# Kernel tuning notes

Measured on AMD Instinct MI355X. Metric: run time of the kernel, lower is better.

## Reference

```python
import jax, jax.numpy as jnp
import numpy as np
import math

B, L, D, A, VD, H = 8, 2048, 1024, 1024, 1024, 1024
EPS = 1e-5

def gelu(x):
    return 0.5 * x * (1.0 + jax.lax.erf(x / math.sqrt(2.0)))

def setup_inputs() -> dict:
    key = jax.random.key(0)
    ks = jax.random.split(key, 12)
    s = 0.02
    return {
        "Q": jax.random.normal(ks[0], (B, L, D), jnp.float32),
        "K": jax.random.normal(ks[1], (B, L, D), jnp.float32),
        "V": jax.random.normal(ks[2], (B, L, D), jnp.float32),
        "attn_mask": jax.random.randint(ks[3], (B, L, L), 0, 2, jnp.int32),
        "Wq": jax.random.normal(ks[4], (D, A), jnp.float32) * s,
        "bq": jnp.zeros((A,), jnp.float32),
        "Wk": jax.random.normal(ks[5], (D, A), jnp.float32) * s,
        "bk": jnp.zeros((A,), jnp.float32),
        "Wv": jax.random.normal(ks[6], (D, VD), jnp.float32) * s,
        "bv": jnp.zeros((VD,), jnp.float32),
        "Wo": jax.random.normal(ks[7], (VD, H), jnp.float32) * s,
        "bo": jnp.zeros((H,), jnp.float32),
        "gamma": jnp.ones((H,), jnp.float32),
        "beta": jnp.zeros((H,), jnp.float32),
    }

def reference(Q, K, V, attn_mask, Wq, bq, Wk, bk, Wv, bv, Wo, bo, gamma, beta):
    q = Q @ Wq + bq                      # [B,L,A]
    k = K @ Wk + bk                      # [B,L,A]
    scores = jnp.einsum('bqa,bka->bqk', q, k) / math.sqrt(A)
    scores = scores + attn_mask.astype(jnp.float32) * (-1e9)
    scores = jnp.swapaxes(scores, -1, -2)  # [B,Lk,Lq]; softmax over QUERY axis
    attn = jax.nn.softmax(scores, axis=-1)
    wv = V @ Wv + bv                     # [B,L,VD]
    context = jnp.einsum('bkq,bqv->bkv', attn, wv)  # [B,L,VD]
    context = gelu(context @ Wo + bo)    # [B,L,H]
    mu = jnp.mean(context, axis=-1, keepdims=True)
    var = jnp.var(context, axis=-1, keepdims=True)
    context = (context - mu) / jnp.sqrt(var + EPS) * gamma + beta
    return context, attn
```

## Files before the change

kernel.cpp:

```cpp
#include <hip/hip_runtime.h>
#include <math.h>

typedef __bf16 bf16;
typedef __bf16 bf16x8 __attribute__((ext_vector_type(8)));
typedef __bf16 bf16x4 __attribute__((ext_vector_type(4)));
typedef float f32x4 __attribute__((ext_vector_type(4)));
typedef unsigned int u32x4 __attribute__((ext_vector_type(4)));

__device__ inline void gload16(const void* g, void* l) {
  typedef __attribute__((address_space(1))) const unsigned int guint;
  typedef __attribute__((address_space(3))) unsigned int luint;
  __builtin_amdgcn_global_load_lds((guint*)g, (luint*)l, 16, 0, 0);
}

template<int BIAS_MODE, bool GELU>
__global__ __launch_bounds__(512, 2)
void bgemm8_k(const bf16* __restrict__ A, const bf16* __restrict__ A2,
              const bf16* __restrict__ B,
              const float* __restrict__ bias, const float* __restrict__ bias2,
              bf16* __restrict__ Cout, int ldc, int K,
              long sAb, long sBb, long sCb, float scale,
              int nshift, int zshift, int mper)
{
  __shared__ __align__(16) char smem[131072];
  bf16* As = (bf16*)smem;
  bf16* Bs = (bf16*)(smem + 65536);

  const int t    = threadIdx.x;
  const int i    = blockIdx.x;
  const int c    = i & 7;
  const int s    = i >> 3;
  const int zb   = c >> zshift;
  const int mchunk = c & ((1 << zshift) - 1);
  const int m_tile = mchunk * mper + (s >> nshift);
  const int n_tile = s & ((1 << nshift) - 1);
  const int m0   = m_tile << 8;
  const int n0   = n_tile << 8;

  const float* bp = (BIAS_MODE && bias2 && zb) ? bias2 : bias;

  const int wave = t >> 6;
  const int lane = t & 63;
  const int wm = wave >> 2;
  const int wn = wave & 3;
  const int fr = lane & 15;
  const int fg = lane >> 4;

  const bf16* Aroot = (A2 && zb >= 4) ? A2 : A;
  const int   za    = (A2 && zb >= 4) ? zb - 4 : zb;
  const bf16* Abase = Aroot + (size_t)za * sAb + (size_t)m0 * K;
  const bf16* Bbase = B + (size_t)zb * sBb + (size_t)n0 * K;
  size_t gOff[2];
  int    ldsOff[2];
#pragma unroll
  for (int j = 0; j < 2; ++j) {
    const int L   = j * 8192 + t * 16;
    const int row = L >> 6;
    const int gp  = (L >> 4) & 3;
    const int g   = gp ^ ((row >> 1) & 3);
    gOff[j]   = (size_t)row * K + (size_t)g * 8;
    ldsOff[j] = j * 4096 + wave * 512;
  }
  const int HMAX = (K >> 5) * 2;

  auto stage = [&](int H) {
    if (H >= HMAX) return;
    const int sl   = H >> 1;
    const int slot = sl & 3;
    const size_t kof = (size_t)sl * 32;
    if ((H & 1) == 0) {
      gload16(Abase + kof + gOff[0], As + slot * 8192 + ldsOff[0]);
      gload16(Abase + kof + gOff[1], As + slot * 8192 + ldsOff[1]);
    } else {
      gload16(Bbase + kof + gOff[0], Bs + slot * 8192 + ldsOff[0]);
      gload16(Bbase + kof + gOff[1], Bs + slot * 8192 + ldsOff[1]);
    }
  };

  const int xsw  = (fg ^ ((fr >> 1) & 3)) * 8;
  const int aoff = (wm * 128 + fr) * 32 + xsw;
  const int boff = (wn * 64 + fr) * 32 + xsw;

  f32x4 acc[8][4] = {};
  const int T = K >> 6;

  stage(0); stage(1); stage(2); stage(3); stage(4);
  asm volatile("s_waitcnt vmcnt(6)" ::: "memory");
  __builtin_amdgcn_s_barrier();

  for (int tt = 0; tt < T; ++tt) {
#pragma unroll
    for (int p = 0; p < 4; ++p) {
      const int kk   = p & 1;
      const int oh   = p >> 1;
      const int slot = (2 * tt + kk) & 3;
      bf16x8 af[4], bfv[4];
#pragma unroll
      for (int i2 = 0; i2 < 4; ++i2)
        af[i2]  = *(const bf16x8*)(As + slot * 8192 + aoff + (oh * 4 + i2) * 512);
#pragma unroll
      for (int i2 = 0; i2 < 4; ++i2)
        bfv[i2] = *(const bf16x8*)(Bs + slot * 8192 + boff + i2 * 512);
      stage(4 * tt + p + 5);
      __builtin_amdgcn_s_barrier();
      __builtin_amdgcn_s_setprio(1);
#pragma unroll
      for (int mi = 0; mi < 4; ++mi)
#pragma unroll
        for (int ni = 0; ni < 4; ++ni)
          acc[oh * 4 + mi][ni] =
            __builtin_amdgcn_mfma_f32_16x16x32_bf16(af[mi], bfv[ni], acc[oh * 4 + mi][ni], 0, 0, 0);
      __builtin_amdgcn_s_setprio(0);
      if (p == 0) {
        if (tt == T - 1) asm volatile("s_waitcnt vmcnt(0)" ::: "memory");
        else             asm volatile("s_waitcnt vmcnt(4)" ::: "memory");
      }
      if (p == 3) {
        if (tt < T - 2)       asm volatile("s_waitcnt vmcnt(6)" ::: "memory");
        else if (tt == T - 2) asm volatile("s_waitcnt vmcnt(4)" ::: "memory");
      }
      __builtin_amdgcn_s_barrier();
    }
  }

  bf16* wbuf = (bf16*)(smem + wave * 16384);
#pragma unroll
  for (int mi = 0; mi < 8; ++mi) {
#pragma unroll
    for (int ni = 0; ni < 4; ++ni) {
      const int col = n0 + wn * 64 + ni * 16 + fr;
#pragma unroll
      for (int i2 = 0; i2 < 4; ++i2) {
        const int r = mi * 16 + fg * 4 + i2;
        float v = acc[mi][ni][i2] * scale;
        if constexpr (BIAS_MODE == 1) v += bp[col];
        if constexpr (BIAS_MODE == 2) v += bp[m0 + wm * 128 + r];
        if constexpr (GELU) v = 0.5f * v * (1.0f + erff(v * 0.70710678118f));
        const int cb = ni * 32 + fr * 2;
        *(bf16*)((char*)wbuf + r * 128 + (cb ^ ((r & 7) << 4))) = (bf16)v;
      }
    }
  }
  __syncthreads();
  const int rowbase = m0 + wm * 128;
  const int colbase = n0 + wn * 64;
#pragma unroll
  for (int j = 0; j < 16; ++j) {
    const int r  = j * 8 + (lane >> 3);
    const int cg = lane & 7;
    bf16x8 val = *(const bf16x8*)((char*)wbuf + r * 128 + ((cg << 4) ^ ((r & 7) << 4)));
    *(bf16x8*)(Cout + (size_t)zb * sCb + (size_t)(rowbase + r) * ldc + colbase + cg * 8) = val;
  }
}

__global__ __launch_bounds__(256)
void pre1_k(const float* __restrict__ W0, const float* __restrict__ W1,
            const float* __restrict__ W2, const float* __restrict__ W3,
            bf16* __restrict__ wts,
            const float* __restrict__ Q, const float* __restrict__ Kin,
            bf16* __restrict__ Qb, bf16* __restrict__ Kb, long n8)
{
  __shared__ __align__(16) char sb[64 * 72 * 2];
  const int t = threadIdx.x;
  if (blockIdx.z == 0) {
    const float* Ws[4] = {W0, W1, W2, W3};
    const int wsel = blockIdx.x >> 8;
    const float* W = Ws[wsel];
    bf16* o = wts + (size_t)wsel * (1024 * 1024);
    const int c0 = (blockIdx.x & 15) * 64;
    const int r0 = ((blockIdx.x >> 4) & 15) * 64;
    bf16 (*tile)[72] = (bf16(*)[72])sb;
    {
      const int rr = t >> 2;
      const int cc = (t & 3) * 16;
      const float* src = W + (size_t)(r0 + rr) * 1024 + c0 + cc;
#pragma unroll
      for (int j = 0; j < 16; j += 4) {
        f32x4 v = __builtin_nontemporal_load((const f32x4*)(src + j));
#pragma unroll
        for (int i = 0; i < 4; ++i) tile[cc + j + i][rr] = (bf16)v[i];
      }
    }
    __syncthreads();
    {
      const int nr = t >> 2;
      const int kc = (t & 3) * 16;
      bf16* dst = o + (size_t)(c0 + nr) * 1024 + r0 + kc;
      *(bf16x8*)dst       = *(const bf16x8*)&tile[nr][kc];
      *(bf16x8*)(dst + 8) = *(const bf16x8*)&tile[nr][kc + 8];
    }
  } else {
    const float* in = (blockIdx.z == 1) ? Q : Kin;
    bf16* out = (blockIdx.z == 1) ? Qb : Kb;
    for (long i = blockIdx.x * 256 + t; i < n8; i += (long)gridDim.x * 256) {
      f32x4 a = __builtin_nontemporal_load((const f32x4*)(in + i * 8));
      f32x4 b = __builtin_nontemporal_load((const f32x4*)(in + i * 8 + 4));
      bf16x8 o;
#pragma unroll
      for (int j = 0; j < 4; ++j) { o[j] = (bf16)a[j]; o[4 + j] = (bf16)b[j]; }
      *(bf16x8*)(out + i * 8) = o;
    }
  }
}

__global__ __launch_bounds__(256)
void pre2_k(const unsigned int* __restrict__ mask, unsigned char* __restrict__ mTb,
            const float* __restrict__ V, bf16* __restrict__ Vb, long n8)
{
  __shared__ __align__(16) char sb[64 * 72 * 2];
  const int t = threadIdx.x;
  if (blockIdx.z < 8) {
    const int b  = blockIdx.z;
    const int k0 = (blockIdx.x & 31) * 64;
    const int q0 = (blockIdx.x >> 5) * 64;
    signed char (*tile)[65] = (signed char(*)[65])sb;
    {
      const int iq = t >> 2;
      const int ic = (t & 3) * 16;
      const unsigned int* src = mask + ((size_t)b * 2048 + q0 + iq) * 2048 + k0 + ic;
#pragma unroll
      for (int j = 0; j < 16; j += 4) {
        u32x4 v = __builtin_nontemporal_load((const u32x4*)(src + j));
#pragma unroll
        for (int i = 0; i < 4; ++i) tile[ic + j + i][iq] = (signed char)v[i];
      }
    }
    __syncthreads();
    {
      const int ik = t >> 2;
      const int iq = (t & 3) * 16;
      unsigned int bits = 0;
#pragma unroll
      for (int j = 0; j < 16; ++j) bits |= (unsigned int)(tile[ik][iq + j] & 1) << j;
      *(unsigned short*)(mTb + ((size_t)b * 2048 + k0 + ik) * 256 + ((q0 + iq) >> 3)) =
          (unsigned short)bits;
    }
  } else {
    for (long i = blockIdx.x * 256 + t; i < n8; i += (long)gridDim.x * 256) {
      f32x4 a = __builtin_nontemporal_load((const f32x4*)(V + i * 8));
      f32x4 b = __builtin_nontemporal_load((const f32x4*)(V + i * 8 + 4));
      bf16x8 o;
#pragma unroll
      for (int j = 0; j < 4; ++j) { o[j] = (bf16)a[j]; o[4 + j] = (bf16)b[j]; }
      *(bf16x8*)(Vb + i * 8) = o;
    }
  }
}

__global__ __launch_bounds__(256)
void softmax_rows_k(float* __restrict__ P, const unsigned char* __restrict__ mTb,
                    bf16* __restrict__ Pb0, bf16* __restrict__ Pb1)
{
  const int b  = blockIdx.x & 7;
  const int rw = blockIdx.x >> 3;
  const size_t r = (size_t)b * 2048 + rw;
  char* slot = (char*)P + r * 8192;
  const bf16* pin = (const bf16*)slot;
  float* pout = (float*)slot;
  bf16* pb = (b < 4) ? (Pb0 + ((size_t)b * 2048 + rw) * 2048)
                     : (Pb1 + ((size_t)(b - 4) * 2048 + rw) * 2048);
  const int t = threadIdx.x;
  const int wave = t >> 6, lane = t & 63;
  bf16x8 raw = *(const bf16x8*)(pin + t * 8);
  const unsigned int mbyte = mTb[r * 256 + t];
  float v[8];
#pragma unroll
  for (int j = 0; j < 8; ++j)
    v[j] = (float)raw[j] + (((mbyte >> j) & 1) ? -1e9f : 0.0f);
  float m = -3e38f;
#pragma unroll
  for (int j = 0; j < 8; ++j) m = fmaxf(m, v[j]);
#pragma unroll
  for (int off = 32; off; off >>= 1) m = fmaxf(m, __shfl_xor(m, off));
  __shared__ float red[8];
  if (lane == 0) red[wave] = m;
  __syncthreads();
  m = fmaxf(fmaxf(red[0], red[1]), fmaxf(red[2], red[3]));
  float s = 0.0f;
#pragma unroll
  for (int j = 0; j < 8; ++j) { v[j] = __expf(v[j] - m); s += v[j]; }
#pragma unroll
  for (int off = 32; off; off >>= 1) s += __shfl_xor(s, off);
  if (lane == 0) red[4 + wave] = s;
  __syncthreads();
  s = red[4] + red[5] + red[6] + red[7];
  const float inv = 1.0f / s;
  f32x4 o0, o1;
  bf16x8 ob;
#pragma unroll
  for (int j = 0; j < 4; ++j) {
    o0[j] = v[j] * inv; o1[j] = v[4 + j] * inv;
    ob[j] = (bf16)o0[j]; ob[4 + j] = (bf16)o1[j];
  }
  __builtin_nontemporal_store(o0, (f32x4*)(pout + t * 8));
  __builtin_nontemporal_store(o1, (f32x4*)(pout + t * 8 + 4));
  *(bf16x8*)(pb + t * 8) = ob;
}

__global__ __launch_bounds__(256)
void ln_k(const bf16* __restrict__ g, const float* __restrict__ gamma,
          const float* __restrict__ beta, float* __restrict__ out)
{
  const size_t r = (size_t)(blockIdx.x & 7) * 2048 + (blockIdx.x >> 3);
  const bf16* p = g + r * 1024;
  const int t = threadIdx.x;
  const int wave = t >> 6, lane = t & 63;
  bf16x4 raw = *(const bf16x4*)(p + t * 4);
  f32x4 v;
#pragma unroll
  for (int j = 0; j < 4; ++j) v[j] = (float)raw[j];
  float s = v[0] + v[1] + v[2] + v[3];
  float q = v[0]*v[0] + v[1]*v[1] + v[2]*v[2] + v[3]*v[3];
#pragma unroll
  for (int off = 32; off; off >>= 1) { s += __shfl_xor(s, off); q += __shfl_xor(q, off); }
  __shared__ float red[16];
  if (lane == 0) { red[wave] = s; red[8 + wave] = q; }
  __syncthreads();
  s = red[0] + red[1] + red[2] + red[3];
  q = red[8] + red[9] + red[10] + red[11];
  const float mu   = s * (1.0f / 1024.0f);
  const float var  = q * (1.0f / 1024.0f) - mu * mu;
  const float rstd = rsqrtf(var + 1e-5f);
  f32x4 gm = *(const f32x4*)(gamma + t * 4);
  f32x4 bt = *(const f32x4*)(beta + t * 4);
  f32x4 o;
#pragma unroll
  for (int j = 0; j < 4; ++j) o[j] = (v[j] - mu) * rstd * gm[j] + bt[j];
  __builtin_nontemporal_store(o, (f32x4*)(out + r * 1024 + t * 4));
}

extern "C" void kernel_launch(void* const* d_in, const int* in_sizes, int n_in,
                              void* d_out, int out_size, void* d_ws, size_t ws_size,
                              hipStream_t stream)
{
  const float* Q     = (const float*)d_in[0];
  const float* Kin   = (const float*)d_in[1];
  const float* V     = (const float*)d_in[2];
  const unsigned int* mask = (const unsigned int*)d_in[3];
  const float* Wq    = (const float*)d_in[4];
  const float* bq    = (const float*)d_in[5];
  const float* Wk    = (const float*)d_in[6];
  const float* bk    = (const float*)d_in[7];
  const float* Wv    = (const float*)d_in[8];
  const float* bv    = (const float*)d_in[9];
  const float* Wo    = (const float*)d_in[10];
  const float* bo    = (const float*)d_in[11];
  const float* gamma = (const float*)d_in[12];
  const float* beta  = (const float*)d_in[13];

  float* outCtx  = (float*)d_out;
  float* outAttn = outCtx + (size_t)8 * 2048 * 1024;

  char* ws = (char*)d_ws;
  const size_t MB = 1048576;
  bf16*          wts   = (bf16*)(ws + 0 * MB);
  bf16*          qp    = (bf16*)(ws + 8 * MB);
  bf16*          kp    = (bf16*)(ws + 40 * MB);
  bf16*          Qb    = (bf16*)(ws + 72 * MB);
  bf16*          Kb    = (bf16*)(ws + 104 * MB);
  unsigned char* mTb   = (unsigned char*)(ws + 72 * MB);
  bf16*          Vb    = (bf16*)(ws + 104 * MB);
  bf16*          wvT   = (bf16*)(ws + 8 * MB);
  bf16*          attnb0= (bf16*)(ws + 40 * MB);
  bf16*          attnb1= (bf16*)(ws + 104 * MB);
  bf16*          ctx   = (bf16*)(ws + 72 * MB);
  bf16*          g     = (bf16*)(ws + 40 * MB);
  bf16* Wvt = wts + 2 * 1024 * 1024;
  bf16* Wot = wts + 3 * 1024 * 1024;

  const dim3 blk(256);
  const dim3 blk8(512);
  const long n8 = (long)16384 * 1024 / 8;

  pre1_k<<<dim3(1024, 1, 3), blk, 0, stream>>>(Wq, Wk, Wv, Wo, wts, Q, Kin, Qb, Kb, n8);
  bgemm8_k<1, false><<<dim3(512), blk8, 0, stream>>>(
      Qb, nullptr, wts, bq, bk, qp, 1024, 1024,
      16777216, 1048576, 16777216, 1.0f, 2, 2, 16);
  pre2_k<<<dim3(1024, 1, 9), blk, 0, stream>>>(mask, mTb, V, Vb, n8);
  bgemm8_k<0, false><<<dim3(512), blk8, 0, stream>>>(
      kp, nullptr, qp, nullptr, nullptr, (bf16*)outAttn, 4096, 1024,
      (long)2048 * 1024, (long)2048 * 1024, (long)2048 * 4096, 0.03125f, 3, 0, 8);
  bgemm8_k<2, false><<<dim3(256), blk8, 0, stream>>>(
      Wvt, nullptr, Vb, bv, nullptr, wvT, 2048, 1024,
      0, (long)2048 * 1024, (long)1024 * 2048, 1.0f, 3, 0, 4);
  softmax_rows_k<<<dim3(16384), blk, 0, stream>>>(outAttn, mTb, attnb0, attnb1);
  bgemm8_k<0, false><<<dim3(256), blk8, 0, stream>>>(
      attnb0, attnb1, wvT, nullptr, nullptr, ctx, 1024, 2048,
      (long)2048 * 2048, (long)1024 * 2048, (long)2048 * 1024, 1.0f, 2, 0, 8);
  bgemm8_k<1, true><<<dim3(256), blk8, 0, stream>>>(
      ctx, nullptr, Wot, bo, nullptr, g, 1024, 1024,
      0, 0, 0, 1.0f, 2, 3, 8);
  ln_k<<<dim3(16384), blk, 0, stream>>>(g, gamma, beta, outCtx);
}
```

Before: 477.4 us.

## Write fp32 attention output from PV GEMM's A-fragments instead of softmax kernel

The softmax kernel now writes only the bf16 probabilities. The fp32 attention output is produced inside the attn@V GEMM: one designated block column per k-slice converts its loaded bf16 A fragments to fp32 and stores them with nontemporal stores. This moves the 128 MB fp32 write out of the memory-bound softmax pass and overlaps it with MFMA work. The returned attn values are now bf16-rounded rather than fp32-precision, and the extra stores in the main loop may disturb the GEMM's vmcnt-based pipelining.

Result: faster. 465.9 us (-2.4%).

```diff
diff --git a/kernel.cpp b/kernel.cpp
--- a/kernel.cpp
+++ b/kernel.cpp
@@ -13,14 +13,15 @@
   __builtin_amdgcn_global_load_lds((guint*)g, (luint*)l, 16, 0, 0);
 }
 
-template<int BIAS_MODE, bool GELU>
+template<int BIAS_MODE, bool GELU, bool PV_ATTN>
 __global__ __launch_bounds__(512, 2)
 void bgemm8_k(const bf16* __restrict__ A, const bf16* __restrict__ A2,
               const bf16* __restrict__ B,
               const float* __restrict__ bias, const float* __restrict__ bias2,
               bf16* __restrict__ Cout, int ldc, int K,
               long sAb, long sBb, long sCb, float scale,
-              int nshift, int zshift, int mper)
+              int nshift, int zshift, int mper,
+              float* __restrict__ attnF, long sFb)
 {
   __shared__ __align__(16) char smem[131072];
   bf16* As = (bf16*)smem;
@@ -111,6 +112,22 @@
           acc[oh * 4 + mi][ni] =
             __builtin_amdgcn_mfma_f32_16x16x32_bf16(af[mi], bfv[ni], acc[oh * 4 + mi][ni], 0, 0, 0);
       __builtin_amdgcn_s_setprio(0);
+      if constexpr (PV_ATTN) {
+        if (wn == 0 && n_tile == (tt >> 3)) {
+          const int sl = 2 * tt + kk;
+          float* fb = attnF + (size_t)zb * sFb
+                    + (size_t)(m0 + wm * 128) * 2048 + sl * 32 + fg * 8;
+#pragma unroll
+          for (int i2 = 0; i2 < 4; ++i2) {
+            const int rloc = (oh * 4 + i2) * 16 + fr;
+            f32x4 lo, hi;
+#pragma unroll
+            for (int e = 0; e < 4; ++e) { lo[e] = (float)af[i2][e]; hi[e] = (float)af[i2][4 + e]; }
+            __builtin_nontemporal_store(lo, (f32x4*)(fb + (size_t)rloc * 2048));
+            __builtin_nontemporal_store(hi, (f32x4*)(fb + (size_t)rloc * 2048 + 4));
+          }
+        }
+      }
       if (p == 0) {
         if (tt == T - 1) asm volatile("s_waitcnt vmcnt(0)" ::: "memory");
         else             asm volatile("s_waitcnt vmcnt(4)" ::: "memory");
@@ -254,9 +271,7 @@
   const int b  = blockIdx.x & 7;
   const int rw = blockIdx.x >> 3;
   const size_t r = (size_t)b * 2048 + rw;
-  char* slot = (char*)P + r * 8192;
-  const bf16* pin = (const bf16*)slot;
-  float* pout = (float*)slot;
+  const bf16* pin = (const bf16*)((const char*)P + r * 8192);
   bf16* pb = (b < 4) ? (Pb0 + ((size_t)b * 2048 + rw) * 2048)
                      : (Pb1 + ((size_t)(b - 4) * 2048 + rw) * 2048);
   const int t = threadIdx.x;
@@ -285,15 +300,9 @@
   __syncthreads();
   s = red[4] + red[5] + red[6] + red[7];
   const float inv = 1.0f / s;
-  f32x4 o0, o1;
   bf16x8 ob;
 #pragma unroll
-  for (int j = 0; j < 4; ++j) {
-    o0[j] = v[j] * inv; o1[j] = v[4 + j] * inv;
-    ob[j] = (bf16)o0[j]; ob[4 + j] = (bf16)o1[j];
-  }
-  __builtin_nontemporal_store(o0, (f32x4*)(pout + t * 8));
-  __builtin_nontemporal_store(o1, (f32x4*)(pout + t * 8 + 4));
+  for (int j = 0; j < 8; ++j) ob[j] = (bf16)(v[j] * inv);
   *(bf16x8*)(pb + t * 8) = ob;
 }
 
@@ -373,22 +382,23 @@
   const long n8 = (long)16384 * 1024 / 8;
 
   pre1_k<<<dim3(1024, 1, 3), blk, 0, stream>>>(Wq, Wk, Wv, Wo, wts, Q, Kin, Qb, Kb, n8);
-  bgemm8_k<1, false><<<dim3(512), blk8, 0, stream>>>(
+  bgemm8_k<1, false, false><<<dim3(512), blk8, 0, stream>>>(
       Qb, nullptr, wts, bq, bk, qp, 1024, 1024,
-      16777216, 1048576, 16777216, 1.0f, 2, 2, 16);
+      16777216, 1048576, 16777216, 1.0f, 2, 2, 16, nullptr, 0);
   pre2_k<<<dim3(1024, 1, 9), blk, 0, stream>>>(mask, mTb, V, Vb, n8);
-  bgemm8_k<0, false><<<dim3(512), blk8, 0, stream>>>(
+  bgemm8_k<0, false, false><<<dim3(512), blk8, 0, stream>>>(
       kp, nullptr, qp, nullptr, nullptr, (bf16*)outAttn, 4096, 1024,
-      (long)2048 * 1024, (long)2048 * 1024, (long)2048 * 4096, 0.03125f, 3, 0, 8);
-  bgemm8_k<2, false><<<dim3(256), blk8, 0, stream>>>(
+      (long)2048 * 1024, (long)2048 * 1024, (long)2048 * 4096, 0.03125f, 3, 0, 8, nullptr, 0);
+  bgemm8_k<2, false, false><<<dim3(256), blk8, 0, stream>>>(
       Wvt, nullptr, Vb, bv, nullptr, wvT, 2048, 1024,
-      0, (long)2048 * 1024, (long)1024 * 2048, 1.0f, 3, 0, 4);
+      0, (long)2048 * 1024, (long)1024 * 2048, 1.0f, 3, 0, 4, nullptr, 0);
   softmax_rows_k<<<dim3(16384), blk, 0, stream>>>(outAttn, mTb, attnb0, attnb1);
-  bgemm8_k<0, false><<<dim3(256), blk8, 0, stream>>>(
+  bgemm8_k<0, false, true><<<dim3(256), blk8, 0, stream>>>(
       attnb0, attnb1, wvT, nullptr, nullptr, ctx, 1024, 2048,
-      (long)2048 * 2048, (long)1024 * 2048, (long)2048 * 1024, 1.0f, 2, 0, 8);
-  bgemm8_k<1, true><<<dim3(256), blk8, 0, stream>>>(
+      (long)2048 * 2048, (long)1024 * 2048, (long)2048 * 1024, 1.0f, 2, 0, 8,
+      outAttn, (long)2048 * 2048);
+  bgemm8_k<1, true, false><<<dim3(256), blk8, 0, stream>>>(
       ctx, nullptr, Wot, bo, nullptr, g, 1024, 1024,
-      0, 0, 0, 1.0f, 2, 3, 8);
+      0, 0, 0, 1.0f, 2, 3, 8, nullptr, 0);
   ln_k<<<dim3(16384), blk, 0, stream>>>(g, gamma, beta, outCtx);
 }
```
